# Optimization experiments

Hardware: AMD Instinct MI355X
Metric: run time of the kernel (lower is better)

Reference implementation:

```python
import jax, jax.numpy as jnp
import numpy as np

B, T = 64, 512
OBS, DM, DS, NL = 115, 128, 8, 3
EMB, NA, H1 = 16, 19, 256


def _ln(x, g, b, eps=1e-5):
    m = jnp.mean(x, -1, keepdims=True)
    v = jnp.mean((x - m) ** 2, -1, keepdims=True)
    return (x - m) * jax.lax.rsqrt(v + eps) * g + b


def _s6(x, h, lng, lnb, w_ig, w_dt, b_dt, a_log, w_b, w_c, d_par, w_out):
    # x: [B,T,DM], h: [B,DM,DS]
    xn = _ln(x, lng, lnb)
    xp = xn @ w_ig.T                               # [B,T,2*DM]
    x_in, z = xp[..., :DM], xp[..., DM:]
    dt = jax.nn.softplus(x_in @ w_dt.T + b_dt)     # [B,T,DM]
    A = -jnp.exp(a_log)                            # [DM,DS]
    bt = x_in @ w_b.T                              # [B,T,DS]
    ct = x_in @ w_c.T                              # [B,T,DS]
    dA = jnp.exp(dt[..., None] * A)                # [B,T,DM,DS]
    upd = (dt * x_in)[..., None] * bt[:, :, None, :]  # [B,T,DM,DS]

    def step(hc, inp):
        dA_t, u_t, c_t = inp
        hn = dA_t * hc + u_t                       # [B,DM,DS]
        y = jnp.einsum('bds,bs->bd', hn, c_t)      # [B,DM]
        return hn, y

    h_f, ys = jax.lax.scan(
        step, h,
        (jnp.swapaxes(dA, 0, 1), jnp.swapaxes(upd, 0, 1), jnp.swapaxes(ct, 0, 1)))
    y = jnp.swapaxes(ys, 0, 1)                     # [B,T,DM]
    ssm = y * jax.nn.silu(z) + x_in * d_par
    return x + ssm @ w_out.T, h_f.reshape(h_f.shape[0], -1)


def _forward(prev_actions, obs, h0, enc_w1, enc_b1, enc_g1, enc_bb1, enc_w2, enc_b2,
             enc_g2, enc_bb2, emb, proj_w, proj_b, proj_g, proj_bb,
             m_ln_g, m_ln_b, m_w_ig, m_w_dt, m_b_dt, m_a_log, m_w_b, m_w_c, m_d, m_w_out,
             fn_g, fn_b, pol_w1, pol_b1, pol_g, pol_bb, pol_w2, pol_b2):
    # MLP encoder: Linear -> LN -> SiLU -> Linear -> LN (final norm)
    e = jax.nn.silu(_ln(obs @ enc_w1.T + enc_b1, enc_g1, enc_bb1))
    e = _ln(e @ enc_w2.T + enc_b2, enc_g2, enc_bb2)
    pa = emb[prev_actions]                         # [B,T,EMB]
    x = jnp.concatenate([e, pa], -1) @ proj_w.T + proj_b
    x = jax.nn.silu(_ln(x, proj_g, proj_bb))
    for i in range(NL):
        x, _ = _s6(x, h0[i].reshape(-1, DM, DS), m_ln_g[i], m_ln_b[i], m_w_ig[i],
                   m_w_dt[i], m_b_dt[i], m_a_log[i], m_w_b[i], m_w_c[i], m_d[i], m_w_out[i])
    x = _ln(x, fn_g, fn_b)
    p = jax.nn.silu(_ln(x @ pol_w1.T + pol_b1, pol_g, pol_bb))
    return p @ pol_w2.T + pol_b2                   # [B,T,NA] policy logits


def setup_inputs() -> dict:
    key = jax.random.key(0)
    ks = iter(jax.random.split(key, 64))
    def n(shape, s=0.05):
        return jax.random.normal(next(ks), shape, dtype=jnp.float32) * s
    return {
        'obs': jax.random.normal(next(ks), (B, T, OBS), dtype=jnp.float32),
        'h0': jnp.zeros((NL, B, DM * DS), jnp.float32),
        'enc_w1': n((H1, OBS)), 'enc_b1': jnp.zeros((H1,)),
        'enc_g1': jnp.ones((H1,)), 'enc_bb1': jnp.zeros((H1,)),
        'enc_w2': n((DM, H1)), 'enc_b2': jnp.zeros((DM,)),
        'enc_g2': jnp.ones((DM,)), 'enc_bb2': jnp.zeros((DM,)),
        'emb': n((NA + 1, EMB), 1.0),
        'proj_w': n((DM, DM + EMB)), 'proj_b': jnp.zeros((DM,)),
        'proj_g': jnp.ones((DM,)), 'proj_bb': jnp.zeros((DM,)),
        'm_ln_g': jnp.ones((NL, DM)), 'm_ln_b': jnp.zeros((NL, DM)),
        'm_w_ig': n((NL, 2 * DM, DM)), 'm_w_dt': n((NL, DM, DM)),
        'm_b_dt': jnp.zeros((NL, DM)),
        'm_a_log': jax.random.uniform(next(ks), (NL, DM, DS), minval=-3.0, maxval=-1.0, dtype=jnp.float32),
        'm_w_b': n((NL, DS, DM)), 'm_w_c': n((NL, DS, DM)),
        'm_d': jnp.ones((NL, DM)), 'm_w_out': n((NL, DM, DM)),
        'fn_g': jnp.ones((DM,)), 'fn_b': jnp.zeros((DM,)),
        'pol_w1': n((DM, DM)), 'pol_b1': jnp.zeros((DM,)),
        'pol_g': jnp.ones((DM,)), 'pol_bb': jnp.zeros((DM,)),
        'pol_w2': n((NA, DM)), 'pol_b2': jnp.zeros((NA,)),
        'prev_actions': jax.random.randint(next(ks), (B, T), 0, NA + 1),
    }


def reference(obs, h0, enc_w1, enc_b1, enc_g1, enc_bb1, enc_w2, enc_b2, enc_g2, enc_bb2,
              emb, proj_w, proj_b, proj_g, proj_bb, m_ln_g, m_ln_b, m_w_ig, m_w_dt,
              m_b_dt, m_a_log, m_w_b, m_w_c, m_d, m_w_out, fn_g, fn_b, pol_w1, pol_b1,
              pol_g, pol_bb, pol_w2, pol_b2, prev_actions):
    return _forward(prev_actions, obs, h0, enc_w1, enc_b1, enc_g1, enc_bb1, enc_w2,
                    enc_b2, enc_g2, enc_bb2, emb, proj_w, proj_b, proj_g, proj_bb,
                    m_ln_g, m_ln_b, m_w_ig, m_w_dt, m_b_dt, m_a_log, m_w_b, m_w_c,
                    m_d, m_w_out, fn_g, fn_b, pol_w1, pol_b1, pol_g, pol_bb, pol_w2, pol_b2)
```

## Files before the change

### kernel.cpp

```cpp
#include <hip/hip_runtime.h>
#include <math.h>

#define BB 64
#define TT 512
#define OBSD 115
#define DMD 128
#define DSD 8
#define NLD 3
#define EMBD 16
#define NAD 19
#define H1D 256
#define NTOK (BB*TT)
#define SSEG 8
#define TSEG (TT/SSEG)

typedef unsigned short ushort_t;
typedef __attribute__((ext_vector_type(8))) short short8;
typedef __attribute__((ext_vector_type(4))) float f32x4;

__device__ __forceinline__ float wsum(float v){
  #pragma unroll
  for (int o = 1; o < 64; o <<= 1) v += __shfl_xor(v, o, 64);
  return v;
}
__device__ __forceinline__ float silu_f(float x){ return x / (1.f + __expf(-x)); }
__device__ __forceinline__ float softplus_f(float x){
  return fmaxf(x, 0.f) + log1pf(__expf(-fabsf(x)));
}
__device__ __forceinline__ ushort_t f2bf(float x){
  unsigned u = __float_as_uint(x);
  unsigned r = (u + 0x7fffu + ((u >> 16) & 1u)) >> 16;
  return (ushort_t)r;
}
__device__ __forceinline__ float b2f(ushort_t x){
  return __uint_as_float(((unsigned)x) << 16);
}
#define MFMA(a,b,c) __builtin_amdgcn_mfma_f32_16x16x32_bf16((a),(b),(c),0,0,0)

struct PJob { const float* src; ushort_t* dst; int N; int K; int Kpad; int rowofs; int Nw; };
struct PJobs { PJob j[20]; };

__global__ __launch_bounds__(256) void k_prep(PJobs P){
  const int job = blockIdx.x >> 2;
  const int sub = blockIdx.x & 3;
  PJob pj = P.j[job];
  const int elems = pj.Nw * pj.Kpad;
  for (int idx = sub*256 + threadIdx.x; idx < elems; idx += 4*256){
    int n = idx / pj.Kpad;
    int k = idx - n*pj.Kpad;
    float v = (n < pj.N && k < pj.K) ? pj.src[(size_t)n*pj.K + k] : 0.f;
    pj.dst[(size_t)(pj.rowofs + n)*pj.Kpad + k] = f2bf(v);
  }
}

__global__ __launch_bounds__(256) void k_enc1(
    const float* __restrict__ obs, const ushort_t* __restrict__ w1b,
    const float* __restrict__ b1, const float* __restrict__ g1,
    const float* __restrict__ bb1, ushort_t* __restrict__ e1)
{
  __shared__ ushort_t s_a[32*136];
  __shared__ float s_val[32*257];
  __shared__ float s_mr[32][2];
  const int tok0 = blockIdx.x * 32;
  const int tid = threadIdx.x;
  const int lane = tid & 63, w = tid >> 6;
  const int q = lane >> 4, cn = lane & 15;
  const int m0 = (w & 1) * 16, nh = w >> 1;

  for (int e = tid; e < 32*16; e += 256){
    int t = e >> 4, kc = e & 15;
    const float* op = obs + (size_t)(tok0 + t)*OBSD;
    short8 v;
    #pragma unroll
    for (int j = 0; j < 8; j++){
      int k = kc*8 + j;
      v[j] = (short)f2bf(k < OBSD ? op[k] : 0.f);
    }
    *(short8*)&s_a[t*136 + kc*8] = v;
  }
  __syncthreads();

  short8 af[4];
  #pragma unroll
  for (int ks = 0; ks < 4; ks++)
    af[ks] = *(const short8*)&s_a[(m0 + cn)*136 + ks*32 + q*8];

  #pragma unroll
  for (int nt = 0; nt < 8; nt++){
    const int n0 = (nh*8 + nt) * 16;
    f32x4 acc = {0.f,0.f,0.f,0.f};
    #pragma unroll
    for (int ks = 0; ks < 4; ks++){
      short8 bf = *(const short8*)&w1b[(size_t)(n0 + cn)*128 + ks*32 + q*8];
      acc = MFMA(af[ks], bf, acc);
    }
    float bias = b1[n0 + cn];
    #pragma unroll
    for (int r = 0; r < 4; r++)
      s_val[(m0 + q*4 + r)*257 + n0 + cn] = acc[r] + bias;
  }
  __syncthreads();

  for (int t = w*8; t < w*8 + 8; t++){
    float v0 = s_val[t*257 + lane],     v1 = s_val[t*257 + lane + 64];
    float v2 = s_val[t*257 + lane+128], v3 = s_val[t*257 + lane + 192];
    float m = wsum(v0+v1+v2+v3) * (1.f/256.f);
    float d0=v0-m, d1=v1-m, d2=v2-m, d3=v3-m;
    float var = wsum(d0*d0+d1*d1+d2*d2+d3*d3) * (1.f/256.f);
    if (lane == 0){ s_mr[t][0] = m; s_mr[t][1] = rsqrtf(var + 1e-5f); }
  }
  __syncthreads();
  for (int e = tid; e < 32*256; e += 256){
    int t = e >> 8, c = e & 255;
    float v = (s_val[t*257 + c] - s_mr[t][0]) * s_mr[t][1] * g1[c] + bb1[c];
    e1[(size_t)(tok0 + t)*256 + c] = f2bf(silu_f(v));
  }
}

__global__ __launch_bounds__(256) void k_enc2p(
    const ushort_t* __restrict__ e1, const ushort_t* __restrict__ w2b,
    const float* __restrict__ b2, const float* __restrict__ g2,
    const float* __restrict__ bb2,
    const float* __restrict__ emb, const int* __restrict__ pact,
    const ushort_t* __restrict__ pwb, const float* __restrict__ pb,
    const float* __restrict__ pg, const float* __restrict__ pbb,
    float* __restrict__ X,
    const float* __restrict__ lng, const float* __restrict__ lnb,
    const ushort_t* __restrict__ wigb, const ushort_t* __restrict__ wdbcb,
    const float* __restrict__ bdt,
    ushort_t* __restrict__ XINo, ushort_t* __restrict__ Zo,
    ushort_t* __restrict__ DTo, float* __restrict__ BTo, float* __restrict__ CTo)
{
  __shared__ float s_val[32*129];
  __shared__ ushort_t s_a[32*168];
  __shared__ ushort_t s_xin[32*136];
  __shared__ float s_mr[32][2];
  const int tok0 = blockIdx.x * 32;
  const int tid = threadIdx.x;
  const int lane = tid & 63, w = tid >> 6;
  const int q = lane >> 4, cn = lane & 15;
  const int m0 = (w & 1) * 16, nh = w >> 1;

  {
    short8 af[8];
    #pragma unroll
    for (int ks = 0; ks < 8; ks++)
      af[ks] = *(const short8*)&e1[(size_t)(tok0 + m0 + cn)*256 + ks*32 + q*8];
    #pragma unroll
    for (int nt = 0; nt < 4; nt++){
      const int n0 = (nh*4 + nt) * 16;
      f32x4 acc = {0.f,0.f,0.f,0.f};
      #pragma unroll
      for (int ks = 0; ks < 8; ks++){
        short8 bf = *(const short8*)&w2b[(size_t)(n0 + cn)*256 + ks*32 + q*8];
        acc = MFMA(af[ks], bf, acc);
      }
      float bias = b2[n0 + cn];
      #pragma unroll
      for (int r = 0; r < 4; r++)
        s_val[(m0 + q*4 + r)*129 + n0 + cn] = acc[r] + bias;
    }
  }
  for (int e = tid; e < 32*32; e += 256){
    int t = e >> 5, k = e & 31;
    float v = 0.f;
    if (k < EMBD){ int a = pact[tok0 + t]; v = emb[(size_t)a*EMBD + k]; }
    s_a[t*168 + 128 + k] = f2bf(v);
  }
  __syncthreads();

  for (int t = w*8; t < w*8 + 8; t++){
    float v0 = s_val[t*129 + lane], v1 = s_val[t*129 + lane + 64];
    float m = wsum(v0+v1) * (1.f/128.f);
    float d0=v0-m, d1=v1-m;
    float var = wsum(d0*d0+d1*d1) * (1.f/128.f);
    if (lane == 0){ s_mr[t][0] = m; s_mr[t][1] = rsqrtf(var + 1e-5f); }
  }
  __syncthreads();
  for (int e = tid; e < 32*128; e += 256){
    int t = e >> 7, c = e & 127;
    float v = (s_val[t*129 + c] - s_mr[t][0]) * s_mr[t][1] * g2[c] + bb2[c];
    s_a[t*168 + c] = f2bf(v);
  }
  __syncthreads();

  {
    short8 af2[5];
    #pragma unroll
    for (int ks = 0; ks < 5; ks++)
      af2[ks] = *(const short8*)&s_a[(m0 + cn)*168 + ks*32 + q*8];
    #pragma unroll
    for (int nt = 0; nt < 4; nt++){
      const int n0 = (nh*4 + nt) * 16;
      f32x4 acc = {0.f,0.f,0.f,0.f};
      #pragma unroll
      for (int ks = 0; ks < 5; ks++){
        short8 bf = *(const short8*)&pwb[(size_t)(n0 + cn)*160 + ks*32 + q*8];
        acc = MFMA(af2[ks], bf, acc);
      }
      float bias = pb[n0 + cn];
      #pragma unroll
      for (int r = 0; r < 4; r++)
        s_val[(m0 + q*4 + r)*129 + n0 + cn] = acc[r] + bias;
    }
  }
  __syncthreads();

  for (int t = w*8; t < w*8 + 8; t++){
    float v0 = s_val[t*129 + lane], v1 = s_val[t*129 + lane + 64];
    float m = wsum(v0+v1) * (1.f/128.f);
    float d0=v0-m, d1=v1-m;
    float var = wsum(d0*d0+d1*d1) * (1.f/128.f);
    if (lane == 0){ s_mr[t][0] = m; s_mr[t][1] = rsqrtf(var + 1e-5f); }
  }
  __syncthreads();
  for (int e = tid; e < 32*128; e += 256){
    int t = e >> 7, c = e & 127;
    float v = (s_val[t*129 + c] - s_mr[t][0]) * s_mr[t][1] * pg[c] + pbb[c];
    v = silu_f(v);
    X[(size_t)tok0*128 + e] = v;
    s_val[t*129 + c] = v;
  }
  __syncthreads();

  for (int t = w*8; t < w*8 + 8; t++){
    float v0 = s_val[t*129 + lane], v1 = s_val[t*129 + lane + 64];
    float m = wsum(v0+v1) * (1.f/128.f);
    float d0=v0-m, d1=v1-m;
    float var = wsum(d0*d0+d1*d1) * (1.f/128.f);
    if (lane == 0){ s_mr[t][0] = m; s_mr[t][1] = rsqrtf(var + 1e-5f); }
  }
  __syncthreads();
  for (int e = tid; e < 32*128; e += 256){
    int t = e >> 7, c = e & 127;
    float v = (s_val[t*129 + c] - s_mr[t][0]) * s_mr[t][1] * lng[c] + lnb[c];
    s_a[t*136 + c] = f2bf(v);
  }
  __syncthreads();

  {
    short8 af[4];
    #pragma unroll
    for (int ks = 0; ks < 4; ks++)
      af[ks] = *(const short8*)&s_a[(m0 + cn)*136 + ks*32 + q*8];
    #pragma unroll
    for (int nt = 0; nt < 8; nt++){
      const int n0 = (nh*8 + nt) * 16;
      f32x4 acc = {0.f,0.f,0.f,0.f};
      #pragma unroll
      for (int ks = 0; ks < 4; ks++){
        short8 bf = *(const short8*)&wigb[(size_t)(n0 + cn)*128 + ks*32 + q*8];
        acc = MFMA(af[ks], bf, acc);
      }
      if (n0 < 128){
        #pragma unroll
        for (int r = 0; r < 4; r++){
          int tr = m0 + q*4 + r;
          ushort_t bb = f2bf(acc[r]);
          XINo[(size_t)(tok0 + tr)*128 + n0 + cn] = bb;
          s_xin[tr*136 + n0 + cn] = bb;
        }
      } else {
        #pragma unroll
        for (int r = 0; r < 4; r++){
          int tr = m0 + q*4 + r;
          Zo[(size_t)(tok0 + tr)*128 + (n0 - 128) + cn] = f2bf(acc[r]);
        }
      }
    }
  }
  __syncthreads();

  {
    short8 af2[4];
    #pragma unroll
    for (int ks = 0; ks < 4; ks++)
      af2[ks] = *(const short8*)&s_xin[(m0 + cn)*136 + ks*32 + q*8];
    for (int nt = nh; nt < 9; nt += 2){
      const int n0 = nt * 16;
      f32x4 acc = {0.f,0.f,0.f,0.f};
      #pragma unroll
      for (int ks = 0; ks < 4; ks++){
        short8 bf = *(const short8*)&wdbcb[(size_t)(n0 + cn)*128 + ks*32 + q*8];
        acc = MFMA(af2[ks], bf, acc);
      }
      const int col = n0 + cn;
      if (col < 128){
        float bd = bdt[col];
        #pragma unroll
        for (int r = 0; r < 4; r++)
          DTo[(size_t)(tok0 + m0 + q*4 + r)*128 + col] = f2bf(softplus_f(acc[r] + bd));
      } else if (col < 136){
        #pragma unroll
        for (int r = 0; r < 4; r++)
          BTo[(size_t)(tok0 + m0 + q*4 + r)*8 + (col - 128)] = acc[r];
      } else {
        #pragma unroll
        for (int r = 0; r < 4; r++)
          CTo[(size_t)(tok0 + m0 + q*4 + r)*8 + (col - 136)] = acc[r];
      }
    }
  }
}

__global__ __launch_bounds__(128) void k_scan1(
    const ushort_t* __restrict__ DTb, const ushort_t* __restrict__ XINb,
    const float* __restrict__ BT, const float* __restrict__ alog,
    float* __restrict__ HLOC, float* __restrict__ PPR)
{
  __shared__ float4 s_bt[TSEG*2];
  const int b  = blockIdx.x >> 3;
  const int sg = blockIdx.x & 7;
  const int d  = threadIdx.x;
  const int t0 = sg * TSEG;

  s_bt[d] = ((const float4*)(BT + ((size_t)b*TT + t0)*8))[d];

  float A2[8], h[8], p[8];
  #pragma unroll
  for (int s = 0; s < 8; s++){
    A2[s] = -__expf(alog[d*8 + s]) * 1.44269504f;
    h[s] = 0.f; p[s] = 1.f;
  }
  __syncthreads();

  const ushort_t* dtp = DTb  + ((size_t)b*TT + t0)*128 + d;
  const ushort_t* xip = XINb + ((size_t)b*TT + t0)*128 + d;

  ushort_t rdt[8], rxi[8], ndt[8], nxi[8];
  #pragma unroll
  for (int r = 0; r < 8; r++){ rdt[r] = dtp[r*128]; rxi[r] = xip[r*128]; }

  for (int c = 0; c < TSEG/8; c++){
    if (c + 1 < TSEG/8){
      #pragma unroll
      for (int r = 0; r < 8; r++){
        ndt[r] = dtp[((c+1)*8 + r)*128];
        nxi[r] = xip[((c+1)*8 + r)*128];
      }
    }
    #pragma unroll
    for (int r = 0; r < 8; r++){
      const int t = c*8 + r;
      float dt = b2f(rdt[r]);
      float wv = dt * b2f(rxi[r]);
      float4 b0 = s_bt[t*2], b1 = s_bt[t*2+1];
      float btv[8] = {b0.x,b0.y,b0.z,b0.w,b1.x,b1.y,b1.z,b1.w};
      #pragma unroll
      for (int s = 0; s < 8; s++){
        float dA = exp2f(dt * A2[s]);
        h[s] = fmaf(dA, h[s], wv * btv[s]);
        p[s] *= dA;
      }
    }
    if (c + 1 < TSEG/8){
      #pragma unroll
      for (int r = 0; r < 8; r++){ rdt[r] = ndt[r]; rxi[r] = nxi[r]; }
    }
  }
  const size_t o = (((size_t)b*SSEG + sg)*128 + d)*8;
  #pragma unroll
  for (int s = 0; s < 8; s++){ HLOC[o+s] = h[s]; PPR[o+s] = p[s]; }
}

__global__ __launch_bounds__(256) void k_carry(
    const float* __restrict__ h0,
    const float* __restrict__ HLOC, const float* __restrict__ PPR,
    float* __restrict__ HST)
{
  const int b = blockIdx.x;
  const int qd = threadIdx.x;
  float4 H = *(const float4*)(h0 + (size_t)b*1024 + qd*4);
  const size_t hb = (size_t)b*SSEG*1024 + qd*4;
  *(float4*)(HST + hb) = H;
  for (int sg = 0; sg < SSEG-1; sg++){
    float4 hl = *(const float4*)(HLOC + hb + (size_t)sg*1024);
    float4 pp = *(const float4*)(PPR  + hb + (size_t)sg*1024);
    H.x = hl.x + pp.x*H.x; H.y = hl.y + pp.y*H.y;
    H.z = hl.z + pp.z*H.z; H.w = hl.w + pp.w*H.w;
    *(float4*)(HST + hb + (size_t)(sg+1)*1024) = H;
  }
}

__device__ __forceinline__ void scan_post_ln(
    const ushort_t* DTb, const ushort_t* XINb, const ushort_t* Zb,
    const float* BT, const float* CT, const float* alog, const float* HST,
    const float* dpar, const ushort_t* woutb, float* X,
    float4* s_bt, float4* s_ct, ushort_t* s_a, float* s_x, float (*s_mr)[2],
    int b, int sg)
{
  const int tid = threadIdx.x;
  const int t0 = sg * TSEG;
  const int d = tid;
  const int lane = tid & 63, w = tid >> 6;
  const int q = lane >> 4, cn = lane & 15;

  s_bt[d] = ((const float4*)(BT + ((size_t)b*TT + t0)*8))[d];
  s_ct[d] = ((const float4*)(CT + ((size_t)b*TT + t0)*8))[d];

  float A2[8], h[8];
  const size_t ho = (((size_t)b*SSEG + sg)*128 + d)*8;
  #pragma unroll
  for (int s = 0; s < 8; s++){
    A2[s] = -__expf(alog[d*8 + s]) * 1.44269504f;
    h[s] = HST[ho + s];
  }
  const float dp = dpar[d];
  __syncthreads();

  const ushort_t* dtp = DTb  + ((size_t)b*TT + t0)*128 + d;
  const ushort_t* xip = XINb + ((size_t)b*TT + t0)*128 + d;
  const ushort_t* zp  = Zb   + ((size_t)b*TT + t0)*128 + d;

  ushort_t rdt[8], rxi[8], rz[8], ndt[8], nxi[8], nz[8];
  #pragma unroll
  for (int r = 0; r < 8; r++){ rdt[r] = dtp[r*128]; rxi[r] = xip[r*128]; rz[r] = zp[r*128]; }

  for (int c = 0; c < TSEG/8; c++){
    if (c + 1 < TSEG/8){
      #pragma unroll
      for (int r = 0; r < 8; r++){
        ndt[r] = dtp[((c+1)*8 + r)*128];
        nxi[r] = xip[((c+1)*8 + r)*128];
        nz[r]  = zp [((c+1)*8 + r)*128];
      }
    }
    #pragma unroll
    for (int r = 0; r < 8; r++){
      const int t = c*8 + r;
      float dt = b2f(rdt[r]);
      float xi = b2f(rxi[r]);
      float wv = dt * xi;
      float4 b0 = s_bt[t*2], b1 = s_bt[t*2+1];
      float4 c0 = s_ct[t*2], c1 = s_ct[t*2+1];
      float btv[8] = {b0.x,b0.y,b0.z,b0.w,b1.x,b1.y,b1.z,b1.w};
      float ctv[8] = {c0.x,c0.y,c0.z,c0.w,c1.x,c1.y,c1.z,c1.w};
      float y = 0.f;
      #pragma unroll
      for (int s = 0; s < 8; s++){
        float dA = exp2f(dt * A2[s]);
        h[s] = fmaf(dA, h[s], wv * btv[s]);
        y = fmaf(h[s], ctv[s], y);
      }
      float ssm = y * silu_f(b2f(rz[r])) + xi * dp;
      s_a[t*136 + d] = f2bf(ssm);
    }
    if (c + 1 < TSEG/8){
      #pragma unroll
      for (int r = 0; r < 8; r++){ rdt[r] = ndt[r]; rxi[r] = nxi[r]; rz[r] = nz[r]; }
    }
  }
  __syncthreads();

  {
    short8 af[4][4];
    #pragma unroll
    for (int mt = 0; mt < 4; mt++)
      #pragma unroll
      for (int ks = 0; ks < 4; ks++)
        af[mt][ks] = *(const short8*)&s_a[(mt*16 + cn)*136 + ks*32 + q*8];

    for (int nt = w; nt < 8; nt += 2){
      const int n0 = nt * 16;
      short8 bf[4];
      #pragma unroll
      for (int ks = 0; ks < 4; ks++)
        bf[ks] = *(const short8*)&woutb[(size_t)(n0 + cn)*128 + ks*32 + q*8];
      #pragma unroll
      for (int mt = 0; mt < 4; mt++){
        f32x4 acc = {0.f,0.f,0.f,0.f};
        #pragma unroll
        for (int ks = 0; ks < 4; ks++) acc = MFMA(af[mt][ks], bf[ks], acc);
        #pragma unroll
        for (int r = 0; r < 4; r++){
          const int tr = mt*16 + q*4 + r;
          const size_t g = ((size_t)b*TT + t0 + tr)*128 + n0 + cn;
          float xn = X[g] + acc[r];
          X[g] = xn;
          s_x[tr*130 + n0 + cn] = xn;
        }
      }
    }
  }
  __syncthreads();

  {
    const int t = tid >> 1, hf = tid & 1;
    float s = 0.f, s2 = 0.f;
    const float* row = s_x + t*130 + hf*64;
    for (int j = 0; j < 64; j++){ float v = row[j]; s += v; s2 = fmaf(v, v, s2); }
    s  += __shfl_xor(s, 1, 64);
    s2 += __shfl_xor(s2, 1, 64);
    float m = s * (1.f/128.f);
    float var = s2 * (1.f/128.f) - m*m;
    if (hf == 0){ s_mr[t][0] = m; s_mr[t][1] = rsqrtf(var + 1e-5f); }
  }
  __syncthreads();
}

__global__ __launch_bounds__(128) void k_scan2p(
    const ushort_t* DTb, const ushort_t* XINb, const ushort_t* Zb,
    const float* __restrict__ BT, const float* __restrict__ CT,
    const float* __restrict__ alog, const float* __restrict__ HST,
    const float* __restrict__ dpar, const ushort_t* __restrict__ woutb,
    float* __restrict__ X,
    const float* __restrict__ lng, const float* __restrict__ lnb,
    const ushort_t* __restrict__ wigb, const ushort_t* __restrict__ wdbcb,
    const float* __restrict__ bdt,
    ushort_t* DToo, ushort_t* XINoo, ushort_t* Zoo,
    float* __restrict__ BTo, float* __restrict__ CTo)
{
  __shared__ float4 s_bt[TSEG*2];
  __shared__ float4 s_ct[TSEG*2];
  __shared__ ushort_t s_a[64*136];
  __shared__ float s_x[64*130];
  __shared__ float s_mr[64][2];

  const int b  = blockIdx.x >> 3;
  const int sg = blockIdx.x & 7;
  const int t0 = sg * TSEG;
  const int tid = threadIdx.x;
  const int lane = tid & 63, w = tid >> 6;
  const int q = lane >> 4, cn = lane & 15;

  scan_post_ln(DTb, XINb, Zb, BT, CT, alog, HST, dpar, woutb, X,
               s_bt, s_ct, s_a, s_x, s_mr, b, sg);

  {
    float g = lng[tid], c = lnb[tid];
    for (int t = 0; t < 64; t++){
      float v = (s_x[t*130 + tid] - s_mr[t][0]) * s_mr[t][1] * g + c;
      s_a[t*136 + tid] = f2bf(v);
    }
  }
  __syncthreads();

  ushort_t* s_xin = (ushort_t*)s_x;

  {
    short8 af[4][4];
    #pragma unroll
    for (int mt = 0; mt < 4; mt++)
      #pragma unroll
      for (int ks = 0; ks < 4; ks++)
        af[mt][ks] = *(const short8*)&s_a[(mt*16 + cn)*136 + ks*32 + q*8];

    for (int nt = w; nt < 16; nt += 2){
      const int n0 = nt * 16;
      short8 bf[4];
      #pragma unroll
      for (int ks = 0; ks < 4; ks++)
        bf[ks] = *(const short8*)&wigb[(size_t)(n0 + cn)*128 + ks*32 + q*8];
      #pragma unroll
      for (int mt = 0; mt < 4; mt++){
        f32x4 acc = {0.f,0.f,0.f,0.f};
        #pragma unroll
        for (int ks = 0; ks < 4; ks++) acc = MFMA(af[mt][ks], bf[ks], acc);
        if (n0 < 128){
          #pragma unroll
          for (int r = 0; r < 4; r++){
            const int tr = mt*16 + q*4 + r;
            ushort_t bb = f2bf(acc[r]);
            XINoo[((size_t)b*TT + t0 + tr)*128 + n0 + cn] = bb;
            s_xin[tr*136 + n0 + cn] = bb;
          }
        } else {
          #pragma unroll
          for (int r = 0; r < 4; r++){
            const int tr = mt*16 + q*4 + r;
            Zoo[((size_t)b*TT + t0 + tr)*128 + (n0 - 128) + cn] = f2bf(acc[r]);
          }
        }
      }
    }
  }
  __syncthreads();

  {
    short8 af[4][4];
    #pragma unroll
    for (int mt = 0; mt < 4; mt++)
      #pragma unroll
      for (int ks = 0; ks < 4; ks++)
        af[mt][ks] = *(const short8*)&s_xin[(mt*16 + cn)*136 + ks*32 + q*8];

    for (int nt = w; nt < 9; nt += 2){
      const int n0 = nt * 16;
      short8 bf[4];
      #pragma unroll
      for (int ks = 0; ks < 4; ks++)
        bf[ks] = *(const short8*)&wdbcb[(size_t)(n0 + cn)*128 + ks*32 + q*8];
      const int col = n0 + cn;
      #pragma unroll
      for (int mt = 0; mt < 4; mt++){
        f32x4 acc = {0.f,0.f,0.f,0.f};
        #pragma unroll
        for (int ks = 0; ks < 4; ks++) acc = MFMA(af[mt][ks], bf[ks], acc);
        if (col < 128){
          float bd = bdt[col];
          #pragma unroll
          for (int r = 0; r < 4; r++)
            DToo[((size_t)b*TT + t0 + mt*16 + q*4 + r)*128 + col] = f2bf(softplus_f(acc[r] + bd));
        } else if (col < 136){
          #pragma unroll
          for (int r = 0; r < 4; r++)
            BTo[((size_t)b*TT + t0 + mt*16 + q*4 + r)*8 + (col - 128)] = acc[r];
        } else {
          #pragma unroll
          for (int r = 0; r < 4; r++)
            CTo[((size_t)b*TT + t0 + mt*16 + q*4 + r)*8 + (col - 136)] = acc[r];
        }
      }
    }
  }
}

__global__ __launch_bounds__(128) void k_scan2h(
    const ushort_t* DTb, const ushort_t* XINb, const ushort_t* Zb,
    const float* __restrict__ BT, const float* __restrict__ CT,
    const float* __restrict__ alog, const float* __restrict__ HST,
    const float* __restrict__ dpar, const ushort_t* __restrict__ woutb,
    float* __restrict__ X,
    const float* __restrict__ fng, const float* __restrict__ fnb,
    const ushort_t* __restrict__ pw1b, const float* __restrict__ pb1,
    const float* __restrict__ pg, const float* __restrict__ pbb,
    const ushort_t* __restrict__ pw2b, const float* __restrict__ pb2,
    float* __restrict__ out)
{
  __shared__ float4 s_bt[TSEG*2];
  __shared__ float4 s_ct[TSEG*2];
  __shared__ ushort_t s_a[64*136];
  __shared__ float s_x[64*130];
  __shared__ float s_mr[64][2];

  const int b  = blockIdx.x >> 3;
  const int sg = blockIdx.x & 7;
  const int t0 = sg * TSEG;
  const int tid = threadIdx.x;
  const int lane = tid & 63, w = tid >> 6;
  const int q = lane >> 4, cn = lane & 15;

  scan_post_ln(DTb, XINb, Zb, BT, CT, alog, HST, dpar, woutb, X,
               s_bt, s_ct, s_a, s_x, s_mr, b, sg);

  {
    float g = fng[tid], c = fnb[tid];
    for (int t = 0; t < 64; t++){
      float v = (s_x[t*130 + tid] - s_mr[t][0]) * s_mr[t][1] * g + c;
      s_a[t*136 + tid] = f2bf(v);
    }
  }
  __syncthreads();

  {
    short8 af[4][4];
    #pragma unroll
    for (int mt = 0; mt < 4; mt++)
      #pragma unroll
      for (int ks = 0; ks < 4; ks++)
        af[mt][ks] = *(const short8*)&s_a[(mt*16 + cn)*136 + ks*32 + q*8];

    for (int nt = w; nt < 8; nt += 2){
      const int n0 = nt * 16;
      short8 bf[4];
      #pragma unroll
      for (int ks = 0; ks < 4; ks++)
        bf[ks] = *(const short8*)&pw1b[(size_t)(n0 + cn)*128 + ks*32 + q*8];
      float bias = pb1[n0 + cn];
      #pragma unroll
      for (int mt = 0; mt < 4; mt++){
        f32x4 acc = {0.f,0.f,0.f,0.f};
        #pragma unroll
        for (int ks = 0; ks < 4; ks++) acc = MFMA(af[mt][ks], bf[ks], acc);
        #pragma unroll
        for (int r = 0; r < 4; r++)
          s_x[(mt*16 + q*4 + r)*130 + n0 + cn] = acc[r] + bias;
      }
    }
  }
  __syncthreads();

  {
    const int t = tid >> 1, hf = tid & 1;
    float s = 0.f, s2 = 0.f;
    const float* row = s_x + t*130 + hf*64;
    for (int j = 0; j < 64; j++){ float v = row[j]; s += v; s2 = fmaf(v, v, s2); }
    s  += __shfl_xor(s, 1, 64);
    s2 += __shfl_xor(s2, 1, 64);
    float m = s * (1.f/128.f);
    float var = s2 * (1.f/128.f) - m*m;
    if (hf == 0){ s_mr[t][0] = m; s_mr[t][1] = rsqrtf(var + 1e-5f); }
  }
  __syncthreads();
  {
    float g = pg[tid], c = pbb[tid];
    for (int t = 0; t < 64; t++){
      float v = (s_x[t*130 + tid] - s_mr[t][0]) * s_mr[t][1] * g + c;
      s_a[t*136 + tid] = f2bf(silu_f(v));
    }
  }
  __syncthreads();

  {
    short8 af[4][4];
    #pragma unroll
    for (int mt = 0; mt < 4; mt++)
      #pragma unroll
      for (int ks = 0; ks < 4; ks++)
        af[mt][ks] = *(const short8*)&s_a[(mt*16 + cn)*136 + ks*32 + q*8];

    const int n0 = w * 16;
    short8 bf[4];
    #pragma unroll
    for (int ks = 0; ks < 4; ks++)
      bf[ks] = *(const short8*)&pw2b[(size_t)(n0 + cn)*128 + ks*32 + q*8];
    const int col = n0 + cn;
    #pragma unroll
    for (int mt = 0; mt < 4; mt++){
      f32x4 acc = {0.f,0.f,0.f,0.f};
      #pragma unroll
      for (int ks = 0; ks < 4; ks++) acc = MFMA(af[mt][ks], bf[ks], acc);
      if (col < NAD){
        float bias = pb2[col];
        #pragma unroll
        for (int r = 0; r < 4; r++)
          out[((size_t)b*TT + t0 + mt*16 + q*4 + r)*NAD + col] = acc[r] + bias;
      }
    }
  }
}

extern "C" void kernel_launch(void* const* d_in, const int* in_sizes, int n_in,
                              void* d_out, int out_size, void* d_ws, size_t ws_size,
                              hipStream_t stream) {
  const float* obs    = (const float*)d_in[0];
  const float* h0     = (const float*)d_in[1];
  const float* enc_w1 = (const float*)d_in[2];
  const float* enc_b1 = (const float*)d_in[3];
  const float* enc_g1 = (const float*)d_in[4];
  const float* enc_bb1= (const float*)d_in[5];
  const float* enc_w2 = (const float*)d_in[6];
  const float* enc_b2 = (const float*)d_in[7];
  const float* enc_g2 = (const float*)d_in[8];
  const float* enc_bb2= (const float*)d_in[9];
  const float* emb    = (const float*)d_in[10];
  const float* proj_w = (const float*)d_in[11];
  const float* proj_b = (const float*)d_in[12];
  const float* proj_g = (const float*)d_in[13];
  const float* proj_bb= (const float*)d_in[14];
  const float* m_ln_g = (const float*)d_in[15];
  const float* m_ln_b = (const float*)d_in[16];
  const float* m_w_ig = (const float*)d_in[17];
  const float* m_w_dt = (const float*)d_in[18];
  const float* m_b_dt = (const float*)d_in[19];
  const float* m_a_log= (const float*)d_in[20];
  const float* m_w_b  = (const float*)d_in[21];
  const float* m_w_c  = (const float*)d_in[22];
  const float* m_d    = (const float*)d_in[23];
  const float* m_w_out= (const float*)d_in[24];
  const float* fn_g   = (const float*)d_in[25];
  const float* fn_b   = (const float*)d_in[26];
  const float* pol_w1 = (const float*)d_in[27];
  const float* pol_b1 = (const float*)d_in[28];
  const float* pol_g  = (const float*)d_in[29];
  const float* pol_bb = (const float*)d_in[30];
  const float* pol_w2 = (const float*)d_in[31];
  const float* pol_b2 = (const float*)d_in[32];
  const int*   pact   = (const int*)d_in[33];

  float* ws  = (float*)d_ws;
  float* X   = ws;
  float* BT  = X  + (size_t)NTOK*128;
  float* CT  = BT + (size_t)NTOK*8;
  float* HLOC= CT + (size_t)NTOK*8;
  float* PPR = HLOC + (size_t)BB*SSEG*1024;
  float* HST = PPR  + (size_t)BB*SSEG*1024;
  ushort_t* E1   = (ushort_t*)(HST + (size_t)BB*SSEG*1024);
  ushort_t* XINb = E1   + (size_t)NTOK*256;
  ushort_t* Zb   = XINb + (size_t)NTOK*128;
  ushort_t* DTb  = Zb   + (size_t)NTOK*128;

  ushort_t* W1B   = DTb   + (size_t)NTOK*128;
  ushort_t* W2B   = W1B   + 256*128;
  ushort_t* PWB   = W2B   + 128*256;
  ushort_t* WIGB  = PWB   + 128*160;
  ushort_t* WDBCB = WIGB  + 3*256*128;
  ushort_t* WOUTB = WDBCB + 3*144*128;
  ushort_t* PW1B  = WOUTB + 3*128*128;
  ushort_t* PW2B  = PW1B  + 128*128;

  PJobs P;
  int nj = 0;
  auto add = [&](const float* src, ushort_t* dst, int N, int K, int Kpad, int rowofs, int Nw){
    P.j[nj].src = src; P.j[nj].dst = dst; P.j[nj].N = N; P.j[nj].K = K;
    P.j[nj].Kpad = Kpad; P.j[nj].rowofs = rowofs; P.j[nj].Nw = Nw; nj++;
  };
  add(enc_w1, W1B, 256, 115, 128, 0, 256);
  add(enc_w2, W2B, 128, 256, 256, 0, 128);
  add(proj_w, PWB, 128, 144, 160, 0, 128);
  for (int l = 0; l < NLD; l++)
    add(m_w_ig + (size_t)l*256*128, WIGB + (size_t)l*256*128, 256, 128, 128, 0, 256);
  for (int l = 0; l < NLD; l++){
    add(m_w_dt + (size_t)l*128*128, WDBCB + (size_t)l*144*128, 128, 128, 128, 0,   128);
    add(m_w_b  + (size_t)l*8*128,   WDBCB + (size_t)l*144*128,   8, 128, 128, 128,   8);
    add(m_w_c  + (size_t)l*8*128,   WDBCB + (size_t)l*144*128,   8, 128, 128, 136,   8);
  }
  for (int l = 0; l < NLD; l++)
    add(m_w_out + (size_t)l*128*128, WOUTB + (size_t)l*128*128, 128, 128, 128, 0, 128);
  add(pol_w1, PW1B, 128, 128, 128, 0, 128);
  add(pol_w2, PW2B,  19, 128, 128, 0,  32);

  k_prep<<<20*4, 256, 0, stream>>>(P);
  k_enc1<<<NTOK/32, 256, 0, stream>>>(obs, W1B, enc_b1, enc_g1, enc_bb1, E1);
  k_enc2p<<<NTOK/32, 256, 0, stream>>>(E1, W2B, enc_b2, enc_g2, enc_bb2,
      emb, pact, PWB, proj_b, proj_g, proj_bb, X,
      m_ln_g, m_ln_b, WIGB, WDBCB, m_b_dt,
      XINb, Zb, DTb, BT, CT);

  for (int l = 0; l < NLD; l++){
    k_scan1<<<BB*SSEG, 128, 0, stream>>>(DTb, XINb, BT,
        m_a_log + (size_t)l*DMD*DSD, HLOC, PPR);
    k_carry<<<BB, 256, 0, stream>>>(h0 + (size_t)l*BB*DMD*DSD, HLOC, PPR, HST);
    if (l < NLD-1){
      int ln = l + 1;
      k_scan2p<<<BB*SSEG, 128, 0, stream>>>(DTb, XINb, Zb, BT, CT,
          m_a_log + (size_t)l*DMD*DSD, HST, m_d + l*128,
          WOUTB + (size_t)l*128*128, X,
          m_ln_g + ln*128, m_ln_b + ln*128,
          WIGB + (size_t)ln*256*128, WDBCB + (size_t)ln*144*128, m_b_dt + ln*128,
          DTb, XINb, Zb, BT, CT);
    } else {
      k_scan2h<<<BB*SSEG, 128, 0, stream>>>(DTb, XINb, Zb, BT, CT,
          m_a_log + (size_t)l*DMD*DSD, HST, m_d + l*128,
          WOUTB + (size_t)l*128*128, X,
          fn_g, fn_b, PW1B, pol_b1, pol_g, pol_bb, PW2B, pol_b2,
          (float*)d_out);
    }
  }
}
```

Before: 449.6 us.

## Fuse encoder kernels and merge chunked scan passes into one block per batch

The two encoder kernels become a single kernel, so the encoder hidden activations stay in shared memory and never make a round trip through global memory. The three scan kernels per layer (local scan, carry, second scan with projection) are merged into one 1024-thread block per batch element that does all eight segments. Inside that block the block-level syncs replace the separate launches, and BT/CT are stored in bf16. This cuts launches and global traffic, but only 64 blocks run the serial scan, so occupancy drops, and the bf16 B/C values lose precision.

```diff
diff --git a/kernel.cpp b/kernel.cpp
--- a/kernel.cpp
+++ b/kernel.cpp
@@ -53,74 +53,12 @@
   }
 }
 
-__global__ __launch_bounds__(256) void k_enc1(
+__global__ __launch_bounds__(256) void k_enc(
     const float* __restrict__ obs, const ushort_t* __restrict__ w1b,
     const float* __restrict__ b1, const float* __restrict__ g1,
-    const float* __restrict__ bb1, ushort_t* __restrict__ e1)
-{
-  __shared__ ushort_t s_a[32*136];
-  __shared__ float s_val[32*257];
-  __shared__ float s_mr[32][2];
-  const int tok0 = blockIdx.x * 32;
-  const int tid = threadIdx.x;
-  const int lane = tid & 63, w = tid >> 6;
-  const int q = lane >> 4, cn = lane & 15;
-  const int m0 = (w & 1) * 16, nh = w >> 1;
-
-  for (int e = tid; e < 32*16; e += 256){
-    int t = e >> 4, kc = e & 15;
-    const float* op = obs + (size_t)(tok0 + t)*OBSD;
-    short8 v;
-    #pragma unroll
-    for (int j = 0; j < 8; j++){
-      int k = kc*8 + j;
-      v[j] = (short)f2bf(k < OBSD ? op[k] : 0.f);
-    }
-    *(short8*)&s_a[t*136 + kc*8] = v;
-  }
-  __syncthreads();
-
-  short8 af[4];
-  #pragma unroll
-  for (int ks = 0; ks < 4; ks++)
-    af[ks] = *(const short8*)&s_a[(m0 + cn)*136 + ks*32 + q*8];
-
-  #pragma unroll
-  for (int nt = 0; nt < 8; nt++){
-    const int n0 = (nh*8 + nt) * 16;
-    f32x4 acc = {0.f,0.f,0.f,0.f};
-    #pragma unroll
-    for (int ks = 0; ks < 4; ks++){
-      short8 bf = *(const short8*)&w1b[(size_t)(n0 + cn)*128 + ks*32 + q*8];
-      acc = MFMA(af[ks], bf, acc);
-    }
-    float bias = b1[n0 + cn];
-    #pragma unroll
-    for (int r = 0; r < 4; r++)
-      s_val[(m0 + q*4 + r)*257 + n0 + cn] = acc[r] + bias;
-  }
-  __syncthreads();
-
-  for (int t = w*8; t < w*8 + 8; t++){
-    float v0 = s_val[t*257 + lane],     v1 = s_val[t*257 + lane + 64];
-    float v2 = s_val[t*257 + lane+128], v3 = s_val[t*257 + lane + 192];
-    float m = wsum(v0+v1+v2+v3) * (1.f/256.f);
-    float d0=v0-m, d1=v1-m, d2=v2-m, d3=v3-m;
-    float var = wsum(d0*d0+d1*d1+d2*d2+d3*d3) * (1.f/256.f);
-    if (lane == 0){ s_mr[t][0] = m; s_mr[t][1] = rsqrtf(var + 1e-5f); }
-  }
-  __syncthreads();
-  for (int e = tid; e < 32*256; e += 256){
-    int t = e >> 8, c = e & 255;
-    float v = (s_val[t*257 + c] - s_mr[t][0]) * s_mr[t][1] * g1[c] + bb1[c];
-    e1[(size_t)(tok0 + t)*256 + c] = f2bf(silu_f(v));
-  }
-}
-
-__global__ __launch_bounds__(256) void k_enc2p(
-    const ushort_t* __restrict__ e1, const ushort_t* __restrict__ w2b,
-    const float* __restrict__ b2, const float* __restrict__ g2,
-    const float* __restrict__ bb2,
+    const float* __restrict__ bb1,
+    const ushort_t* __restrict__ w2b, const float* __restrict__ b2,
+    const float* __restrict__ g2, const float* __restrict__ bb2,
     const float* __restrict__ emb, const int* __restrict__ pact,
     const ushort_t* __restrict__ pwb, const float* __restrict__ pb,
     const float* __restrict__ pg, const float* __restrict__ pbb,
@@ -128,45 +66,101 @@
     const float* __restrict__ lng, const float* __restrict__ lnb,
     const ushort_t* __restrict__ wigb, const ushort_t* __restrict__ wdbcb,
     const float* __restrict__ bdt,
-    ushort_t* __restrict__ XINo, ushort_t* __restrict__ Zo,
-    ushort_t* __restrict__ DTo, float* __restrict__ BTo, float* __restrict__ CTo)
+    ushort_t* __restrict__ XINb, ushort_t* __restrict__ Zb,
+    ushort_t* __restrict__ DTb, ushort_t* __restrict__ BTu, ushort_t* __restrict__ CTu)
 {
-  __shared__ float s_val[32*129];
-  __shared__ ushort_t s_a[32*168];
-  __shared__ ushort_t s_xin[32*136];
-  __shared__ float s_mr[32][2];
+  __shared__ __align__(16) char sm[58752];
+  float*    s_val257 = (float*)sm;
+  ushort_t* s_e1     = (ushort_t*)(sm + 32896);
+  ushort_t* s_obs    = (ushort_t*)(sm + 49792);
+  float*    s_mr     = (float*)(sm + 58496);
+  ushort_t* s_a      = (ushort_t*)sm;
+  float*    s_val    = (float*)(sm + 10752);
+  ushort_t* s_xin    = (ushort_t*)(sm + 32896);
+
   const int tok0 = blockIdx.x * 32;
   const int tid = threadIdx.x;
   const int lane = tid & 63, w = tid >> 6;
   const int q = lane >> 4, cn = lane & 15;
   const int m0 = (w & 1) * 16, nh = w >> 1;
 
-  {
-    short8 af[8];
-    #pragma unroll
-    for (int ks = 0; ks < 8; ks++)
-      af[ks] = *(const short8*)&e1[(size_t)(tok0 + m0 + cn)*256 + ks*32 + q*8];
-    #pragma unroll
-    for (int nt = 0; nt < 4; nt++){
-      const int n0 = (nh*4 + nt) * 16;
+  for (int e = tid; e < 32*16; e += 256){
+    int t = e >> 4, kc = e & 15;
+    const float* op = obs + (size_t)(tok0 + t)*OBSD;
+    short8 v;
+    #pragma unroll
+    for (int j = 0; j < 8; j++){
+      int k = kc*8 + j;
+      v[j] = (short)f2bf(k < OBSD ? op[k] : 0.f);
+    }
+    *(short8*)&s_obs[t*136 + kc*8] = v;
+  }
+  __syncthreads();
+
+  {
+    short8 af[4];
+    #pragma unroll
+    for (int ks = 0; ks < 4; ks++)
+      af[ks] = *(const short8*)&s_obs[(m0 + cn)*136 + ks*32 + q*8];
+    #pragma unroll
+    for (int nt = 0; nt < 8; nt++){
+      const int n0 = (nh*8 + nt) * 16;
       f32x4 acc = {0.f,0.f,0.f,0.f};
       #pragma unroll
-      for (int ks = 0; ks < 8; ks++){
-        short8 bf = *(const short8*)&w2b[(size_t)(n0 + cn)*256 + ks*32 + q*8];
+      for (int ks = 0; ks < 4; ks++){
+        short8 bf = *(const short8*)&w1b[(size_t)(n0 + cn)*128 + ks*32 + q*8];
         acc = MFMA(af[ks], bf, acc);
       }
-      float bias = b2[n0 + cn];
+      float bias = b1[n0 + cn];
       #pragma unroll
       for (int r = 0; r < 4; r++)
-        s_val[(m0 + q*4 + r)*129 + n0 + cn] = acc[r] + bias;
-    }
-  }
+        s_val257[(m0 + q*4 + r)*257 + n0 + cn] = acc[r] + bias;
+    }
+  }
+  __syncthreads();
+
+  for (int t = w*8; t < w*8 + 8; t++){
+    float v0 = s_val257[t*257 + lane],     v1 = s_val257[t*257 + lane + 64];
+    float v2 = s_val257[t*257 + lane+128], v3 = s_val257[t*257 + lane + 192];
+    float m = wsum(v0+v1+v2+v3) * (1.f/256.f);
+    float d0=v0-m, d1=v1-m, d2=v2-m, d3=v3-m;
+    float var = wsum(d0*d0+d1*d1+d2*d2+d3*d3) * (1.f/256.f);
+    if (lane == 0){ s_mr[t*2] = m; s_mr[t*2+1] = rsqrtf(var + 1e-5f); }
+  }
+  __syncthreads();
+  for (int e = tid; e < 32*256; e += 256){
+    int t = e >> 8, c = e & 255;
+    float v = (s_val257[t*257 + c] - s_mr[t*2]) * s_mr[t*2+1] * g1[c] + bb1[c];
+    s_e1[t*264 + c] = f2bf(silu_f(v));
+  }
+  __syncthreads();
+
   for (int e = tid; e < 32*32; e += 256){
     int t = e >> 5, k = e & 31;
     float v = 0.f;
     if (k < EMBD){ int a = pact[tok0 + t]; v = emb[(size_t)a*EMBD + k]; }
     s_a[t*168 + 128 + k] = f2bf(v);
   }
+  {
+    short8 af[8];
+    #pragma unroll
+    for (int ks = 0; ks < 8; ks++)
+      af[ks] = *(const short8*)&s_e1[(m0 + cn)*264 + ks*32 + q*8];
+    #pragma unroll
+    for (int nt = 0; nt < 4; nt++){
+      const int n0 = (nh*4 + nt) * 16;
+      f32x4 acc = {0.f,0.f,0.f,0.f};
+      #pragma unroll
+      for (int ks = 0; ks < 8; ks++){
+        short8 bf = *(const short8*)&w2b[(size_t)(n0 + cn)*256 + ks*32 + q*8];
+        acc = MFMA(af[ks], bf, acc);
+      }
+      float bias = b2[n0 + cn];
+      #pragma unroll
+      for (int r = 0; r < 4; r++)
+        s_val[(m0 + q*4 + r)*129 + n0 + cn] = acc[r] + bias;
+    }
+  }
   __syncthreads();
 
   for (int t = w*8; t < w*8 + 8; t++){
@@ -174,12 +168,12 @@
     float m = wsum(v0+v1) * (1.f/128.f);
     float d0=v0-m, d1=v1-m;
     float var = wsum(d0*d0+d1*d1) * (1.f/128.f);
-    if (lane == 0){ s_mr[t][0] = m; s_mr[t][1] = rsqrtf(var + 1e-5f); }
+    if (lane == 0){ s_mr[t*2] = m; s_mr[t*2+1] = rsqrtf(var + 1e-5f); }
   }
   __syncthreads();
   for (int e = tid; e < 32*128; e += 256){
     int t = e >> 7, c = e & 127;
-    float v = (s_val[t*129 + c] - s_mr[t][0]) * s_mr[t][1] * g2[c] + bb2[c];
+    float v = (s_val[t*129 + c] - s_mr[t*2]) * s_mr[t*2+1] * g2[c] + bb2[c];
     s_a[t*168 + c] = f2bf(v);
   }
   __syncthreads();
@@ -211,12 +205,12 @@
     float m = wsum(v0+v1) * (1.f/128.f);
     float d0=v0-m, d1=v1-m;
     float var = wsum(d0*d0+d1*d1) * (1.f/128.f);
-    if (lane == 0){ s_mr[t][0] = m; s_mr[t][1] = rsqrtf(var + 1e-5f); }
+    if (lane == 0){ s_mr[t*2] = m; s_mr[t*2+1] = rsqrtf(var + 1e-5f); }
   }
   __syncthreads();
   for (int e = tid; e < 32*128; e += 256){
     int t = e >> 7, c = e & 127;
-    float v = (s_val[t*129 + c] - s_mr[t][0]) * s_mr[t][1] * pg[c] + pbb[c];
+    float v = (s_val[t*129 + c] - s_mr[t*2]) * s_mr[t*2+1] * pg[c] + pbb[c];
     v = silu_f(v);
     X[(size_t)tok0*128 + e] = v;
     s_val[t*129 + c] = v;
@@ -228,13 +222,13 @@
     float m = wsum(v0+v1) * (1.f/128.f);
     float d0=v0-m, d1=v1-m;
     float var = wsum(d0*d0+d1*d1) * (1.f/128.f);
-    if (lane == 0){ s_mr[t][0] = m; s_mr[t][1] = rsqrtf(var + 1e-5f); }
+    if (lane == 0){ s_mr[t*2] = m; s_mr[t*2+1] = rsqrtf(var + 1e-5f); }
   }
   __syncthreads();
   for (int e = tid; e < 32*128; e += 256){
     int t = e >> 7, c = e & 127;
-    float v = (s_val[t*129 + c] - s_mr[t][0]) * s_mr[t][1] * lng[c] + lnb[c];
-    s_a[t*136 + c] = f2bf(v);
+    float v = (s_val[t*129 + c] - s_mr[t*2]) * s_mr[t*2+1] * lng[c] + lnb[c];
+    s_a[t*168 + c] = f2bf(v);
   }
   __syncthreads();
 
@@ -242,7 +236,7 @@
     short8 af[4];
     #pragma unroll
     for (int ks = 0; ks < 4; ks++)
-      af[ks] = *(const short8*)&s_a[(m0 + cn)*136 + ks*32 + q*8];
+      af[ks] = *(const short8*)&s_a[(m0 + cn)*168 + ks*32 + q*8];
     #pragma unroll
     for (int nt = 0; nt < 8; nt++){
       const int n0 = (nh*8 + nt) * 16;
@@ -257,14 +251,14 @@
         for (int r = 0; r < 4; r++){
           int tr = m0 + q*4 + r;
           ushort_t bb = f2bf(acc[r]);
-          XINo[(size_t)(tok0 + tr)*128 + n0 + cn] = bb;
+          XINb[(size_t)(tok0 + tr)*128 + n0 + cn] = bb;
           s_xin[tr*136 + n0 + cn] = bb;
         }
       } else {
         #pragma unroll
         for (int r = 0; r < 4; r++){
           int tr = m0 + q*4 + r;
-          Zo[(size_t)(tok0 + tr)*128 + (n0 - 128) + cn] = f2bf(acc[r]);
+          Zb[(size_t)(tok0 + tr)*128 + (n0 - 128) + cn] = f2bf(acc[r]);
         }
       }
     }
@@ -289,444 +283,388 @@
         float bd = bdt[col];
         #pragma unroll
         for (int r = 0; r < 4; r++)
-          DTo[(size_t)(tok0 + m0 + q*4 + r)*128 + col] = f2bf(softplus_f(acc[r] + bd));
+          DTb[(size_t)(tok0 + m0 + q*4 + r)*128 + col] = f2bf(softplus_f(acc[r] + bd));
       } else if (col < 136){
         #pragma unroll
         for (int r = 0; r < 4; r++)
-          BTo[(size_t)(tok0 + m0 + q*4 + r)*8 + (col - 128)] = acc[r];
+          BTu[(size_t)(tok0 + m0 + q*4 + r)*8 + (col - 128)] = f2bf(acc[r]);
       } else {
         #pragma unroll
         for (int r = 0; r < 4; r++)
-          CTo[(size_t)(tok0 + m0 + q*4 + r)*8 + (col - 136)] = acc[r];
-      }
-    }
-  }
-}
-
-__global__ __launch_bounds__(128) void k_scan1(
+          CTu[(size_t)(tok0 + m0 + q*4 + r)*8 + (col - 136)] = f2bf(acc[r]);
+      }
+    }
+  }
+}
+
+__device__ void scan_all(
     const ushort_t* __restrict__ DTb, const ushort_t* __restrict__ XINb,
-    const float* __restrict__ BT, const float* __restrict__ alog,
-    float* __restrict__ HLOC, float* __restrict__ PPR)
-{
-  __shared__ float4 s_bt[TSEG*2];
-  const int b  = blockIdx.x >> 3;
-  const int sg = blockIdx.x & 7;
-  const int d  = threadIdx.x;
-  const int t0 = sg * TSEG;
-
-  s_bt[d] = ((const float4*)(BT + ((size_t)b*TT + t0)*8))[d];
-
-  float A2[8], h[8], p[8];
-  #pragma unroll
-  for (int s = 0; s < 8; s++){
-    A2[s] = -__expf(alog[d*8 + s]) * 1.44269504f;
-    h[s] = 0.f; p[s] = 1.f;
-  }
-  __syncthreads();
-
-  const ushort_t* dtp = DTb  + ((size_t)b*TT + t0)*128 + d;
-  const ushort_t* xip = XINb + ((size_t)b*TT + t0)*128 + d;
-
-  ushort_t rdt[8], rxi[8], ndt[8], nxi[8];
-  #pragma unroll
-  for (int r = 0; r < 8; r++){ rdt[r] = dtp[r*128]; rxi[r] = xip[r*128]; }
-
-  for (int c = 0; c < TSEG/8; c++){
-    if (c + 1 < TSEG/8){
-      #pragma unroll
-      for (int r = 0; r < 8; r++){
-        ndt[r] = dtp[((c+1)*8 + r)*128];
-        nxi[r] = xip[((c+1)*8 + r)*128];
-      }
-    }
-    #pragma unroll
-    for (int r = 0; r < 8; r++){
-      const int t = c*8 + r;
-      float dt = b2f(rdt[r]);
-      float wv = dt * b2f(rxi[r]);
-      float4 b0 = s_bt[t*2], b1 = s_bt[t*2+1];
-      float btv[8] = {b0.x,b0.y,b0.z,b0.w,b1.x,b1.y,b1.z,b1.w};
-      #pragma unroll
-      for (int s = 0; s < 8; s++){
-        float dA = exp2f(dt * A2[s]);
-        h[s] = fmaf(dA, h[s], wv * btv[s]);
-        p[s] *= dA;
-      }
-    }
-    if (c + 1 < TSEG/8){
-      #pragma unroll
-      for (int r = 0; r < 8; r++){ rdt[r] = ndt[r]; rxi[r] = nxi[r]; }
-    }
-  }
-  const size_t o = (((size_t)b*SSEG + sg)*128 + d)*8;
-  #pragma unroll
-  for (int s = 0; s < 8; s++){ HLOC[o+s] = h[s]; PPR[o+s] = p[s]; }
-}
-
-__global__ __launch_bounds__(256) void k_carry(
-    const float* __restrict__ h0,
-    const float* __restrict__ HLOC, const float* __restrict__ PPR,
-    float* __restrict__ HST)
-{
-  const int b = blockIdx.x;
-  const int qd = threadIdx.x;
-  float4 H = *(const float4*)(h0 + (size_t)b*1024 + qd*4);
-  const size_t hb = (size_t)b*SSEG*1024 + qd*4;
-  *(float4*)(HST + hb) = H;
-  for (int sg = 0; sg < SSEG-1; sg++){
-    float4 hl = *(const float4*)(HLOC + hb + (size_t)sg*1024);
-    float4 pp = *(const float4*)(PPR  + hb + (size_t)sg*1024);
-    H.x = hl.x + pp.x*H.x; H.y = hl.y + pp.y*H.y;
-    H.z = hl.z + pp.z*H.z; H.w = hl.w + pp.w*H.w;
-    *(float4*)(HST + hb + (size_t)(sg+1)*1024) = H;
-  }
-}
-
-__device__ __forceinline__ void scan_post_ln(
-    const ushort_t* DTb, const ushort_t* XINb, const ushort_t* Zb,
-    const float* BT, const float* CT, const float* alog, const float* HST,
-    const float* dpar, const ushort_t* woutb, float* X,
-    float4* s_bt, float4* s_ct, ushort_t* s_a, float* s_x, float (*s_mr)[2],
-    int b, int sg)
+    const ushort_t* __restrict__ Zb,
+    const ushort_t* __restrict__ BTu, const ushort_t* __restrict__ CTu,
+    const float* __restrict__ alog, const float* __restrict__ h0g,
+    const float* __restrict__ dpar,
+    float* __restrict__ HLOC, float* __restrict__ PPR,
+    ushort_t* __restrict__ SSMg,
+    ushort_t* s_bt, ushort_t* s_ct, float* s_hst, int b)
 {
   const int tid = threadIdx.x;
-  const int t0 = sg * TSEG;
-  const int d = tid;
-  const int lane = tid & 63, w = tid >> 6;
-  const int q = lane >> 4, cn = lane & 15;
-
-  s_bt[d] = ((const float4*)(BT + ((size_t)b*TT + t0)*8))[d];
-  s_ct[d] = ((const float4*)(CT + ((size_t)b*TT + t0)*8))[d];
-
-  float A2[8], h[8];
-  const size_t ho = (((size_t)b*SSEG + sg)*128 + d)*8;
+  const int sg = tid >> 7, d = tid & 127;
+
+  if (tid < 512){
+    ((uint4*)s_bt)[tid] = ((const uint4*)(BTu + (size_t)b*TT*8))[tid];
+    ((uint4*)s_ct)[tid] = ((const uint4*)(CTu + (size_t)b*TT*8))[tid];
+  }
+  float A2[8];
   #pragma unroll
-  for (int s = 0; s < 8; s++){
-    A2[s] = -__expf(alog[d*8 + s]) * 1.44269504f;
-    h[s] = HST[ho + s];
-  }
-  const float dp = dpar[d];
-  __syncthreads();
-
-  const ushort_t* dtp = DTb  + ((size_t)b*TT + t0)*128 + d;
-  const ushort_t* xip = XINb + ((size_t)b*TT + t0)*128 + d;
-  const ushort_t* zp  = Zb   + ((size_t)b*TT + t0)*128 + d;
-
-  ushort_t rdt[8], rxi[8], rz[8], ndt[8], nxi[8], nz[8];
+  for (int s = 0; s < 8; s++) A2[s] = -__expf(alog[d*8+s]) * 1.44269504f;
+  __syncthreads();
+
+  const size_t rowbase = ((size_t)b*TT + sg*TSEG)*128 + d;
+  const ushort_t* dtp = DTb + rowbase;
+  const ushort_t* xip = XINb + rowbase;
+
+  {
+    float h[8], p[8];
+    #pragma unroll
+    for (int s = 0; s < 8; s++){ h[s]=0.f; p[s]=1.f; }
+    ushort_t rdt[8], rxi[8], ndt[8], nxi[8];
+    #pragma unroll
+    for (int r = 0; r < 8; r++){ rdt[r]=dtp[r*128]; rxi[r]=xip[r*128]; }
+    for (int c = 0; c < 8; c++){
+      if (c < 7){
+        #pragma unroll
+        for (int r = 0; r < 8; r++){
+          ndt[r]=dtp[((c+1)*8+r)*128]; nxi[r]=xip[((c+1)*8+r)*128];
+        }
+      }
+      #pragma unroll
+      for (int r = 0; r < 8; r++){
+        const int t = c*8 + r;
+        float dt = b2f(rdt[r]);
+        float wv = dt * b2f(rxi[r]);
+        const ushort_t* bro = &s_bt[(sg*TSEG + t)*8];
+        #pragma unroll
+        for (int s = 0; s < 8; s++){
+          float dA = exp2f(dt * A2[s]);
+          h[s] = fmaf(dA, h[s], wv * b2f(bro[s]));
+          p[s] *= dA;
+        }
+      }
+      if (c < 7){
+        #pragma unroll
+        for (int r = 0; r < 8; r++){ rdt[r]=ndt[r]; rxi[r]=nxi[r]; }
+      }
+    }
+    const size_t o = (((size_t)b*8 + sg)*1024) + d*8;
+    #pragma unroll
+    for (int s = 0; s < 8; s++){ HLOC[o+s]=h[s]; PPR[o+s]=p[s]; }
+  }
+  __threadfence_block();
+  __syncthreads();
+
+  {
+    float H = h0g[(size_t)b*1024 + tid];
+    const size_t cb = (size_t)b*8*1024 + tid;
+    #pragma unroll
+    for (int sgi = 0; sgi < 8; sgi++){
+      float hl = HLOC[cb + (size_t)sgi*1024];
+      float pp = PPR [cb + (size_t)sgi*1024];
+      s_hst[sgi*1024 + tid] = H;
+      H = fmaf(pp, H, hl);
+    }
+  }
+  __syncthreads();
+
+  {
+    const ushort_t* zp = Zb + rowbase;
+    float h[8];
+    #pragma unroll
+    for (int s = 0; s < 8; s++) h[s] = s_hst[sg*1024 + d*8 + s];
+    const float dp = dpar[d];
+    ushort_t rdt[8], rxi[8], rz[8], ndt[8], nxi[8], nz[8];
+    #pragma unroll
+    for (int r = 0; r < 8; r++){ rdt[r]=dtp[r*128]; rxi[r]=xip[r*128]; rz[r]=zp[r*128]; }
+    for (int c = 0; c < 8; c++){
+      if (c < 7){
+        #pragma unroll
+        for (int r = 0; r < 8; r++){
+          ndt[r]=dtp[((c+1)*8+r)*128]; nxi[r]=xip[((c+1)*8+r)*128]; nz[r]=zp[((c+1)*8+r)*128];
+        }
+      }
+      #pragma unroll
+      for (int r = 0; r < 8; r++){
+        const int t = c*8 + r;
+        float dt = b2f(rdt[r]);
+        float xi = b2f(rxi[r]);
+        float wv = dt * xi;
+        const ushort_t* bro = &s_bt[(sg*TSEG + t)*8];
+        const ushort_t* cro = &s_ct[(sg*TSEG + t)*8];
+        float y = 0.f;
+        #pragma unroll
+        for (int s = 0; s < 8; s++){
+          float dA = exp2f(dt * A2[s]);
+          h[s] = fmaf(dA, h[s], wv * b2f(bro[s]));
+          y = fmaf(h[s], b2f(cro[s]), y);
+        }
+        float ssm = y * silu_f(b2f(rz[r])) + xi * dp;
+        SSMg[rowbase + t*128] = f2bf(ssm);
+      }
+      if (c < 7){
+        #pragma unroll
+        for (int r = 0; r < 8; r++){ rdt[r]=ndt[r]; rxi[r]=nxi[r]; rz[r]=nz[r]; }
+      }
+    }
+  }
+}
+
+__device__ __forceinline__ void postC_wout(
+    const ushort_t* __restrict__ SSMg, const ushort_t* __restrict__ woutb,
+    float* __restrict__ X, ushort_t* s_a, float* s_x, int b, int sgc)
+{
+  const int tid = threadIdx.x;
+  {
+    const unsigned* src = (const unsigned*)(SSMg + ((size_t)b*TT + sgc*TSEG)*128);
+    for (int i = tid; i < 4096; i += 1024){
+      int t = i >> 6, cp = i & 63;
+      *(unsigned*)&s_a[t*136 + cp*2] = src[i];
+    }
+  }
+  __syncthreads();
+  const int w = tid >> 6, lane = tid & 63, q = lane >> 4, cn = lane & 15;
+  const int nt = w & 7, mt0 = w >> 3;
+  const int n0 = nt*16;
+  short8 bf[4];
   #pragma unroll
-  for (int r = 0; r < 8; r++){ rdt[r] = dtp[r*128]; rxi[r] = xip[r*128]; rz[r] = zp[r*128]; }
-
-  for (int c = 0; c < TSEG/8; c++){
-    if (c + 1 < TSEG/8){
-      #pragma unroll
-      for (int r = 0; r < 8; r++){
-        ndt[r] = dtp[((c+1)*8 + r)*128];
-        nxi[r] = xip[((c+1)*8 + r)*128];
-        nz[r]  = zp [((c+1)*8 + r)*128];
-      }
-    }
-    #pragma unroll
-    for (int r = 0; r < 8; r++){
-      const int t = c*8 + r;
-      float dt = b2f(rdt[r]);
-      float xi = b2f(rxi[r]);
-      float wv = dt * xi;
-      float4 b0 = s_bt[t*2], b1 = s_bt[t*2+1];
-      float4 c0 = s_ct[t*2], c1 = s_ct[t*2+1];
-      float btv[8] = {b0.x,b0.y,b0.z,b0.w,b1.x,b1.y,b1.z,b1.w};
-      float ctv[8] = {c0.x,c0.y,c0.z,c0.w,c1.x,c1.y,c1.z,c1.w};
-      float y = 0.f;
-      #pragma unroll
-      for (int s = 0; s < 8; s++){
-        float dA = exp2f(dt * A2[s]);
-        h[s] = fmaf(dA, h[s], wv * btv[s]);
-        y = fmaf(h[s], ctv[s], y);
-      }
-      float ssm = y * silu_f(b2f(rz[r])) + xi * dp;
-      s_a[t*136 + d] = f2bf(ssm);
-    }
-    if (c + 1 < TSEG/8){
-      #pragma unroll
-      for (int r = 0; r < 8; r++){ rdt[r] = ndt[r]; rxi[r] = nxi[r]; rz[r] = nz[r]; }
-    }
-  }
-  __syncthreads();
-
-  {
-    short8 af[4][4];
-    #pragma unroll
-    for (int mt = 0; mt < 4; mt++)
-      #pragma unroll
-      for (int ks = 0; ks < 4; ks++)
-        af[mt][ks] = *(const short8*)&s_a[(mt*16 + cn)*136 + ks*32 + q*8];
-
-    for (int nt = w; nt < 8; nt += 2){
-      const int n0 = nt * 16;
-      short8 bf[4];
-      #pragma unroll
-      for (int ks = 0; ks < 4; ks++)
-        bf[ks] = *(const short8*)&woutb[(size_t)(n0 + cn)*128 + ks*32 + q*8];
-      #pragma unroll
-      for (int mt = 0; mt < 4; mt++){
-        f32x4 acc = {0.f,0.f,0.f,0.f};
-        #pragma unroll
-        for (int ks = 0; ks < 4; ks++) acc = MFMA(af[mt][ks], bf[ks], acc);
-        #pragma unroll
-        for (int r = 0; r < 4; r++){
-          const int tr = mt*16 + q*4 + r;
-          const size_t g = ((size_t)b*TT + t0 + tr)*128 + n0 + cn;
-          float xn = X[g] + acc[r];
-          X[g] = xn;
-          s_x[tr*130 + n0 + cn] = xn;
-        }
-      }
-    }
-  }
-  __syncthreads();
-
-  {
-    const int t = tid >> 1, hf = tid & 1;
-    float s = 0.f, s2 = 0.f;
-    const float* row = s_x + t*130 + hf*64;
-    for (int j = 0; j < 64; j++){ float v = row[j]; s += v; s2 = fmaf(v, v, s2); }
-    s  += __shfl_xor(s, 1, 64);
-    s2 += __shfl_xor(s2, 1, 64);
-    float m = s * (1.f/128.f);
-    float var = s2 * (1.f/128.f) - m*m;
-    if (hf == 0){ s_mr[t][0] = m; s_mr[t][1] = rsqrtf(var + 1e-5f); }
-  }
-  __syncthreads();
-}
-
-__global__ __launch_bounds__(128) void k_scan2p(
-    const ushort_t* DTb, const ushort_t* XINb, const ushort_t* Zb,
-    const float* __restrict__ BT, const float* __restrict__ CT,
-    const float* __restrict__ alog, const float* __restrict__ HST,
+  for (int ks = 0; ks < 4; ks++)
+    bf[ks] = *(const short8*)&woutb[(size_t)(n0+cn)*128 + ks*32 + q*8];
+  #pragma unroll
+  for (int mi = 0; mi < 2; mi++){
+    const int mt = mt0 + mi*2;
+    short8 af[4];
+    #pragma unroll
+    for (int ks = 0; ks < 4; ks++)
+      af[ks] = *(const short8*)&s_a[(mt*16+cn)*136 + ks*32 + q*8];
+    f32x4 acc = {0.f,0.f,0.f,0.f};
+    #pragma unroll
+    for (int ks = 0; ks < 4; ks++) acc = MFMA(af[ks], bf[ks], acc);
+    #pragma unroll
+    for (int r = 0; r < 4; r++){
+      const int tr = mt*16 + q*4 + r;
+      const size_t g = ((size_t)b*TT + sgc*TSEG + tr)*128 + n0 + cn;
+      float xn = X[g] + acc[r];
+      X[g] = xn;
+      s_x[tr*130 + n0 + cn] = xn;
+    }
+  }
+  __syncthreads();
+}
+
+__device__ __forceinline__ void lnC(const float* s_x, ushort_t* s_a,
+    const float* __restrict__ gv, const float* __restrict__ bv, bool dosilu)
+{
+  const int tid = threadIdx.x;
+  const int t = tid >> 4, part = tid & 15;
+  const float* row = s_x + t*130 + part*8;
+  float s = 0.f, s2 = 0.f;
+  #pragma unroll
+  for (int j = 0; j < 8; j++){ float v = row[j]; s += v; s2 = fmaf(v, v, s2); }
+  #pragma unroll
+  for (int o = 1; o < 16; o <<= 1){ s += __shfl_xor(s, o, 64); s2 += __shfl_xor(s2, o, 64); }
+  float m = s * (1.f/128.f);
+  float rstd = rsqrtf(s2*(1.f/128.f) - m*m + 1e-5f);
+  #pragma unroll
+  for (int j = 0; j < 8; j++){
+    int c = part*8 + j;
+    float v = (row[j] - m) * rstd * gv[c] + bv[c];
+    if (dosilu) v = silu_f(v);
+    s_a[t*136 + c] = f2bf(v);
+  }
+}
+
+__global__ __launch_bounds__(1024) void k_scanF_p(
+    ushort_t* DTb, ushort_t* XINb, ushort_t* Zb,
+    ushort_t* BTu, ushort_t* CTu,
+    const float* __restrict__ alog, const float* __restrict__ h0g,
     const float* __restrict__ dpar, const ushort_t* __restrict__ woutb,
     float* __restrict__ X,
+    float* __restrict__ HLOC, float* __restrict__ PPR,
+    ushort_t* __restrict__ SSMg,
     const float* __restrict__ lng, const float* __restrict__ lnb,
     const ushort_t* __restrict__ wigb, const ushort_t* __restrict__ wdbcb,
-    const float* __restrict__ bdt,
-    ushort_t* DToo, ushort_t* XINoo, ushort_t* Zoo,
-    float* __restrict__ BTo, float* __restrict__ CTo)
+    const float* __restrict__ bdt)
 {
-  __shared__ float4 s_bt[TSEG*2];
-  __shared__ float4 s_ct[TSEG*2];
-  __shared__ ushort_t s_a[64*136];
-  __shared__ float s_x[64*130];
-  __shared__ float s_mr[64][2];
-
-  const int b  = blockIdx.x >> 3;
-  const int sg = blockIdx.x & 7;
-  const int t0 = sg * TSEG;
+  __shared__ __align__(16) char sm[51200];
+  ushort_t* s_bt = (ushort_t*)sm;
+  ushort_t* s_ct = (ushort_t*)(sm + 8192);
+  float*    s_hst= (float*)(sm + 16384);
+  const int b = blockIdx.x;
+
+  scan_all(DTb, XINb, Zb, BTu, CTu, alog, h0g, dpar, HLOC, PPR, SSMg,
+           s_bt, s_ct, s_hst, b);
+  __syncthreads();
+
+  ushort_t* s_a   = (ushort_t*)sm;
+  float*    s_x   = (float*)(sm + 17408);
+  ushort_t* s_xin = (ushort_t*)(sm + 17408);
+
   const int tid = threadIdx.x;
-  const int lane = tid & 63, w = tid >> 6;
-  const int q = lane >> 4, cn = lane & 15;
-
-  scan_post_ln(DTb, XINb, Zb, BT, CT, alog, HST, dpar, woutb, X,
-               s_bt, s_ct, s_a, s_x, s_mr, b, sg);
-
-  {
-    float g = lng[tid], c = lnb[tid];
-    for (int t = 0; t < 64; t++){
-      float v = (s_x[t*130 + tid] - s_mr[t][0]) * s_mr[t][1] * g + c;
-      s_a[t*136 + tid] = f2bf(v);
-    }
-  }
-  __syncthreads();
-
-  ushort_t* s_xin = (ushort_t*)s_x;
-
-  {
-    short8 af[4][4];
-    #pragma unroll
-    for (int mt = 0; mt < 4; mt++)
+  const int w = tid >> 6, lane = tid & 63, q = lane >> 4, cn = lane & 15;
+
+  for (int sgc = 0; sgc < 8; sgc++){
+    postC_wout(SSMg, woutb, X, s_a, s_x, b, sgc);
+    lnC(s_x, s_a, lng, lnb, false);
+    __syncthreads();
+
+    {
+      const int n0 = w * 16;
+      short8 bf[4];
       #pragma unroll
       for (int ks = 0; ks < 4; ks++)
-        af[mt][ks] = *(const short8*)&s_a[(mt*16 + cn)*136 + ks*32 + q*8];
-
-    for (int nt = w; nt < 16; nt += 2){
-      const int n0 = nt * 16;
-      short8 bf[4];
-      #pragma unroll
-      for (int ks = 0; ks < 4; ks++)
-        bf[ks] = *(const short8*)&wigb[(size_t)(n0 + cn)*128 + ks*32 + q*8];
+        bf[ks] = *(const short8*)&wigb[(size_t)(n0+cn)*128 + ks*32 + q*8];
       #pragma unroll
       for (int mt = 0; mt < 4; mt++){
+        short8 af[4];
+        #pragma unroll
+        for (int ks = 0; ks < 4; ks++)
+          af[ks] = *(const short8*)&s_a[(mt*16+cn)*136 + ks*32 + q*8];
         f32x4 acc = {0.f,0.f,0.f,0.f};
         #pragma unroll
-        for (int ks = 0; ks < 4; ks++) acc = MFMA(af[mt][ks], bf[ks], acc);
+        for (int ks = 0; ks < 4; ks++) acc = MFMA(af[ks], bf[ks], acc);
         if (n0 < 128){
           #pragma unroll
           for (int r = 0; r < 4; r++){
             const int tr = mt*16 + q*4 + r;
             ushort_t bb = f2bf(acc[r]);
-            XINoo[((size_t)b*TT + t0 + tr)*128 + n0 + cn] = bb;
+            XINb[((size_t)b*TT + sgc*TSEG + tr)*128 + n0 + cn] = bb;
             s_xin[tr*136 + n0 + cn] = bb;
           }
         } else {
           #pragma unroll
           for (int r = 0; r < 4; r++){
             const int tr = mt*16 + q*4 + r;
-            Zoo[((size_t)b*TT + t0 + tr)*128 + (n0 - 128) + cn] = f2bf(acc[r]);
+            Zb[((size_t)b*TT + sgc*TSEG + tr)*128 + (n0-128) + cn] = f2bf(acc[r]);
           }
         }
       }
     }
-  }
-  __syncthreads();
-
-  {
-    short8 af[4][4];
-    #pragma unroll
-    for (int mt = 0; mt < 4; mt++)
-      #pragma unroll
-      for (int ks = 0; ks < 4; ks++)
-        af[mt][ks] = *(const short8*)&s_xin[(mt*16 + cn)*136 + ks*32 + q*8];
-
-    for (int nt = w; nt < 9; nt += 2){
+    __syncthreads();
+
+    for (int task = w; task < 36; task += 16){
+      const int nt = task >> 2, mt = task & 3;
       const int n0 = nt * 16;
-      short8 bf[4];
-      #pragma unroll
-      for (int ks = 0; ks < 4; ks++)
-        bf[ks] = *(const short8*)&wdbcb[(size_t)(n0 + cn)*128 + ks*32 + q*8];
+      short8 bf[4], af[4];
+      #pragma unroll
+      for (int ks = 0; ks < 4; ks++){
+        bf[ks] = *(const short8*)&wdbcb[(size_t)(n0+cn)*128 + ks*32 + q*8];
+        af[ks] = *(const short8*)&s_xin[(mt*16+cn)*136 + ks*32 + q*8];
+      }
+      f32x4 acc = {0.f,0.f,0.f,0.f};
+      #pragma unroll
+      for (int ks = 0; ks < 4; ks++) acc = MFMA(af[ks], bf[ks], acc);
       const int col = n0 + cn;
-      #pragma unroll
-      for (int mt = 0; mt < 4; mt++){
-        f32x4 acc = {0.f,0.f,0.f,0.f};
-        #pragma unroll
-        for (int ks = 0; ks < 4; ks++) acc = MFMA(af[mt][ks], bf[ks], acc);
-        if (col < 128){
-          float bd = bdt[col];
-          #pragma unroll
-          for (int r = 0; r < 4; r++)
-            DToo[((size_t)b*TT + t0 + mt*16 + q*4 + r)*128 + col] = f2bf(softplus_f(acc[r] + bd));
-        } else if (col < 136){
-          #pragma unroll
-          for (int r = 0; r < 4; r++)
-            BTo[((size_t)b*TT + t0 + mt*16 + q*4 + r)*8 + (col - 128)] = acc[r];
-        } else {
-          #pragma unroll
-          for (int r = 0; r < 4; r++)
-            CTo[((size_t)b*TT + t0 + mt*16 + q*4 + r)*8 + (col - 136)] = acc[r];
-        }
-      }
-    }
-  }
-}
-
-__global__ __launch_bounds__(128) void k_scan2h(
+      if (col < 128){
+        float bd = bdt[col];
+        #pragma unroll
+        for (int r = 0; r < 4; r++)
+          DTb[((size_t)b*TT + sgc*TSEG + mt*16 + q*4 + r)*128 + col] = f2bf(softplus_f(acc[r] + bd));
+      } else if (col < 136){
+        #pragma unroll
+        for (int r = 0; r < 4; r++)
+          BTu[((size_t)b*TT + sgc*TSEG + mt*16 + q*4 + r)*8 + (col-128)] = f2bf(acc[r]);
+      } else {
+        #pragma unroll
+        for (int r = 0; r < 4; r++)
+          CTu[((size_t)b*TT + sgc*TSEG + mt*16 + q*4 + r)*8 + (col-136)] = f2bf(acc[r]);
+      }
+    }
+    __syncthreads();
+  }
+}
+
+__global__ __launch_bounds__(1024) void k_scanF_h(
     const ushort_t* DTb, const ushort_t* XINb, const ushort_t* Zb,
-    const float* __restrict__ BT, const float* __restrict__ CT,
-    const float* __restrict__ alog, const float* __restrict__ HST,
+    const ushort_t* __restrict__ BTu, const ushort_t* __restrict__ CTu,
+    const float* __restrict__ alog, const float* __restrict__ h0g,
     const float* __restrict__ dpar, const ushort_t* __restrict__ woutb,
     float* __restrict__ X,
+    float* __restrict__ HLOC, float* __restrict__ PPR,
+    ushort_t* __restrict__ SSMg,
     const float* __restrict__ fng, const float* __restrict__ fnb,
     const ushort_t* __restrict__ pw1b, const float* __restrict__ pb1,
     const float* __restrict__ pg, const float* __restrict__ pbb,
     const ushort_t* __restrict__ pw2b, const float* __restrict__ pb2,
     float* __restrict__ out)
 {
-  __shared__ float4 s_bt[TSEG*2];
-  __shared__ float4 s_ct[TSEG*2];
-  __shared__ ushort_t s_a[64*136];
-  __shared__ float s_x[64*130];
-  __shared__ float s_mr[64][2];
-
-  const int b  = blockIdx.x >> 3;
-  const int sg = blockIdx.x & 7;
-  const int t0 = sg * TSEG;
+  __shared__ __align__(16) char sm[51200];
+  ushort_t* s_bt = (ushort_t*)sm;
+  ushort_t* s_ct = (ushort_t*)(sm + 8192);
+  float*    s_hst= (float*)(sm + 16384);
+  const int b = blockIdx.x;
+
+  scan_all(DTb, XINb, Zb, BTu, CTu, alog, h0g, dpar, HLOC, PPR, SSMg,
+           s_bt, s_ct, s_hst, b);
+  __syncthreads();
+
+  ushort_t* s_a = (ushort_t*)sm;
+  float*    s_x = (float*)(sm + 17408);
+
   const int tid = threadIdx.x;
-  const int lane = tid & 63, w = tid >> 6;
-  const int q = lane >> 4, cn = lane & 15;
-
-  scan_post_ln(DTb, XINb, Zb, BT, CT, alog, HST, dpar, woutb, X,
-               s_bt, s_ct, s_a, s_x, s_mr, b, sg);
-
-  {
-    float g = fng[tid], c = fnb[tid];
-    for (int t = 0; t < 64; t++){
-      float v = (s_x[t*130 + tid] - s_mr[t][0]) * s_mr[t][1] * g + c;
-      s_a[t*136 + tid] = f2bf(v);
-    }
-  }
-  __syncthreads();
-
-  {
-    short8 af[4][4];
-    #pragma unroll
-    for (int mt = 0; mt < 4; mt++)
-      #pragma unroll
-      for (int ks = 0; ks < 4; ks++)
-        af[mt][ks] = *(const short8*)&s_a[(mt*16 + cn)*136 + ks*32 + q*8];
-
-    for (int nt = w; nt < 8; nt += 2){
+  const int w = tid >> 6, lane = tid & 63, q = lane >> 4, cn = lane & 15;
+
+  for (int sgc = 0; sgc < 8; sgc++){
+    postC_wout(SSMg, woutb, X, s_a, s_x, b, sgc);
+    lnC(s_x, s_a, fng, fnb, false);
+    __syncthreads();
+
+    {
+      const int nt = w & 7, mt0 = w >> 3;
       const int n0 = nt * 16;
       short8 bf[4];
       #pragma unroll
       for (int ks = 0; ks < 4; ks++)
-        bf[ks] = *(const short8*)&pw1b[(size_t)(n0 + cn)*128 + ks*32 + q*8];
+        bf[ks] = *(const short8*)&pw1b[(size_t)(n0+cn)*128 + ks*32 + q*8];
       float bias = pb1[n0 + cn];
       #pragma unroll
-      for (int mt = 0; mt < 4; mt++){
+      for (int mi = 0; mi < 2; mi++){
+        const int mt = mt0 + mi*2;
+        short8 af[4];
+        #pragma unroll
+        for (int ks = 0; ks < 4; ks++)
+          af[ks] = *(const short8*)&s_a[(mt*16+cn)*136 + ks*32 + q*8];
         f32x4 acc = {0.f,0.f,0.f,0.f};
         #pragma unroll
-        for (int ks = 0; ks < 4; ks++) acc = MFMA(af[mt][ks], bf[ks], acc);
+        for (int ks = 0; ks < 4; ks++) acc = MFMA(af[ks], bf[ks], acc);
         #pragma unroll
         for (int r = 0; r < 4; r++)
           s_x[(mt*16 + q*4 + r)*130 + n0 + cn] = acc[r] + bias;
       }
     }
-  }
-  __syncthreads();
-
-  {
-    const int t = tid >> 1, hf = tid & 1;
-    float s = 0.f, s2 = 0.f;
-    const float* row = s_x + t*130 + hf*64;
-    for (int j = 0; j < 64; j++){ float v = row[j]; s += v; s2 = fmaf(v, v, s2); }
-    s  += __shfl_xor(s, 1, 64);
-    s2 += __shfl_xor(s2, 1, 64);
-    float m = s * (1.f/128.f);
-    float var = s2 * (1.f/128.f) - m*m;
-    if (hf == 0){ s_mr[t][0] = m; s_mr[t][1] = rsqrtf(var + 1e-5f); }
-  }
-  __syncthreads();
-  {
-    float g = pg[tid], c = pbb[tid];
-    for (int t = 0; t < 64; t++){
-      float v = (s_x[t*130 + tid] - s_mr[t][0]) * s_mr[t][1] * g + c;
-      s_a[t*136 + tid] = f2bf(silu_f(v));
-    }
-  }
-  __syncthreads();
-
-  {
-    short8 af[4][4];
-    #pragma unroll
-    for (int mt = 0; mt < 4; mt++)
-      #pragma unroll
-      for (int ks = 0; ks < 4; ks++)
-        af[mt][ks] = *(const short8*)&s_a[(mt*16 + cn)*136 + ks*32 + q*8];
-
-    const int n0 = w * 16;
-    short8 bf[4];
-    #pragma unroll
-    for (int ks = 0; ks < 4; ks++)
-      bf[ks] = *(const short8*)&pw2b[(size_t)(n0 + cn)*128 + ks*32 + q*8];
-    const int col = n0 + cn;
-    #pragma unroll
-    for (int mt = 0; mt < 4; mt++){
+    __syncthreads();
+
+    lnC(s_x, s_a, pg, pbb, true);
+    __syncthreads();
+
+    if (w < 8){
+      const int nt = w >> 2, mt = w & 3;
+      const int n0 = nt * 16;
+      short8 bf[4], af[4];
+      #pragma unroll
+      for (int ks = 0; ks < 4; ks++){
+        bf[ks] = *(const short8*)&pw2b[(size_t)(n0+cn)*128 + ks*32 + q*8];
+        af[ks] = *(const short8*)&s_a[(mt*16+cn)*136 + ks*32 + q*8];
+      }
       f32x4 acc = {0.f,0.f,0.f,0.f};
       #pragma unroll
-      for (int ks = 0; ks < 4; ks++) acc = MFMA(af[mt][ks], bf[ks], acc);
+      for (int ks = 0; ks < 4; ks++) acc = MFMA(af[ks], bf[ks], acc);
+      const int col = n0 + cn;
       if (col < NAD){
         float bias = pb2[col];
         #pragma unroll
         for (int r = 0; r < 4; r++)
-          out[((size_t)b*TT + t0 + mt*16 + q*4 + r)*NAD + col] = acc[r] + bias;
-      }
-    }
+          out[((size_t)b*TT + sgc*TSEG + mt*16 + q*4 + r)*NAD + col] = acc[r] + bias;
+      }
+    }
+    __syncthreads();
   }
 }
 
@@ -769,18 +707,17 @@
   const int*   pact   = (const int*)d_in[33];
 
   float* ws  = (float*)d_ws;
-  float* X   = ws;
-  float* BT  = X  + (size_t)NTOK*128;
-  float* CT  = BT + (size_t)NTOK*8;
-  float* HLOC= CT + (size_t)NTOK*8;
-  float* PPR = HLOC + (size_t)BB*SSEG*1024;
-  float* HST = PPR  + (size_t)BB*SSEG*1024;
-  ushort_t* E1   = (ushort_t*)(HST + (size_t)BB*SSEG*1024);
-  ushort_t* XINb = E1   + (size_t)NTOK*256;
+  float* X    = ws;
+  float* HLOC = X + (size_t)NTOK*128;
+  float* PPR  = HLOC + (size_t)BB*8*1024;
+  ushort_t* XINb = (ushort_t*)(PPR + (size_t)BB*8*1024);
   ushort_t* Zb   = XINb + (size_t)NTOK*128;
   ushort_t* DTb  = Zb   + (size_t)NTOK*128;
-
-  ushort_t* W1B   = DTb   + (size_t)NTOK*128;
+  ushort_t* SSMg = DTb  + (size_t)NTOK*128;
+  ushort_t* BTu  = SSMg + (size_t)NTOK*128;
+  ushort_t* CTu  = BTu  + (size_t)NTOK*8;
+
+  ushort_t* W1B   = CTu   + (size_t)NTOK*8;
   ushort_t* W2B   = W1B   + 256*128;
   ushort_t* PWB   = W2B   + 128*256;
   ushort_t* WIGB  = PWB   + 128*160;
@@ -811,30 +748,23 @@
   add(pol_w2, PW2B,  19, 128, 128, 0,  32);
 
   k_prep<<<20*4, 256, 0, stream>>>(P);
-  k_enc1<<<NTOK/32, 256, 0, stream>>>(obs, W1B, enc_b1, enc_g1, enc_bb1, E1);
-  k_enc2p<<<NTOK/32, 256, 0, stream>>>(E1, W2B, enc_b2, enc_g2, enc_bb2,
-      emb, pact, PWB, proj_b, proj_g, proj_bb, X,
+  k_enc<<<NTOK/32, 256, 0, stream>>>(obs, W1B, enc_b1, enc_g1, enc_bb1,
+      W2B, enc_b2, enc_g2, enc_bb2, emb, pact,
+      PWB, proj_b, proj_g, proj_bb, X,
       m_ln_g, m_ln_b, WIGB, WDBCB, m_b_dt,
-      XINb, Zb, DTb, BT, CT);
-
-  for (int l = 0; l < NLD; l++){
-    k_scan1<<<BB*SSEG, 128, 0, stream>>>(DTb, XINb, BT,
-        m_a_log + (size_t)l*DMD*DSD, HLOC, PPR);
-    k_carry<<<BB, 256, 0, stream>>>(h0 + (size_t)l*BB*DMD*DSD, HLOC, PPR, HST);
-    if (l < NLD-1){
-      int ln = l + 1;
-      k_scan2p<<<BB*SSEG, 128, 0, stream>>>(DTb, XINb, Zb, BT, CT,
-          m_a_log + (size_t)l*DMD*DSD, HST, m_d + l*128,
-          WOUTB + (size_t)l*128*128, X,
-          m_ln_g + ln*128, m_ln_b + ln*128,
-          WIGB + (size_t)ln*256*128, WDBCB + (size_t)ln*144*128, m_b_dt + ln*128,
-          DTb, XINb, Zb, BT, CT);
-    } else {
-      k_scan2h<<<BB*SSEG, 128, 0, stream>>>(DTb, XINb, Zb, BT, CT,
-          m_a_log + (size_t)l*DMD*DSD, HST, m_d + l*128,
-          WOUTB + (size_t)l*128*128, X,
-          fn_g, fn_b, PW1B, pol_b1, pol_g, pol_bb, PW2B, pol_b2,
-          (float*)d_out);
-    }
-  }
-}
+      XINb, Zb, DTb, BTu, CTu);
+
+  for (int l = 0; l < NLD-1; l++){
+    int ln = l + 1;
+    k_scanF_p<<<BB, 1024, 0, stream>>>(DTb, XINb, Zb, BTu, CTu,
+        m_a_log + (size_t)l*DMD*DSD, h0 + (size_t)l*BB*1024, m_d + l*128,
+        WOUTB + (size_t)l*128*128, X, HLOC, PPR, SSMg,
+        m_ln_g + ln*128, m_ln_b + ln*128,
+        WIGB + (size_t)ln*256*128, WDBCB + (size_t)ln*144*128, m_b_dt + ln*128);
+  }
+  k_scanF_h<<<BB, 1024, 0, stream>>>(DTb, XINb, Zb, BTu, CTu,
+      m_a_log + (size_t)2*DMD*DSD, h0 + (size_t)2*BB*1024, m_d + 2*128,
+      WOUTB + (size_t)2*128*128, X, HLOC, PPR, SSMg,
+      fn_g, fn_b, PW1B, pol_b1, pol_g, pol_bb, PW2B, pol_b2,
+      (float*)d_out);
+}
```

After: 1.296 ms. +188.2%, slower.
